# Optimization experiments

Hardware: AMD Instinct MI355X
Metric: run time of the kernel (lower is better)

Reference implementation:

```python
import jax, jax.numpy as jnp
import numpy as np

N_NODES = 50000
N_EDGES = 800000
G_DIM = 128
H1_DIM = 128
H2_DIM = 128
N_REL = 8          # 2 * n_speakers**2, n_speakers = 2
N_BASES = 30


def setup_inputs() -> dict:
    key = jax.random.key(0)
    ks = jax.random.split(key, 10)
    node_features = jax.random.normal(ks[0], (N_NODES, G_DIM), jnp.float32)
    edge_index = jax.random.randint(ks[1], (2, N_EDGES), 0, N_NODES, jnp.int32)
    edge_norm = jax.random.uniform(ks[2], (N_EDGES,), jnp.float32)
    edge_type = jax.random.randint(ks[3], (N_EDGES,), 0, N_REL, jnp.int32)
    # RGCN basis-decomposition params
    w_comp = jax.random.normal(ks[4], (N_REL, N_BASES), jnp.float32) / np.sqrt(N_BASES)
    bases = jax.random.normal(ks[5], (N_BASES, G_DIM, H1_DIM), jnp.float32) / np.sqrt(G_DIM)
    loop_weight = jax.random.normal(ks[6], (G_DIM, H1_DIM), jnp.float32) / np.sqrt(G_DIM)
    bias1 = jnp.zeros((H1_DIM,), jnp.float32)
    # GraphConv params
    W2 = jax.random.normal(ks[7], (H1_DIM, H2_DIM), jnp.float32) / np.sqrt(H1_DIM)
    bias2 = jnp.zeros((H2_DIM,), jnp.float32)
    return dict(node_features=node_features, edge_index=edge_index,
                edge_norm=edge_norm, edge_type=edge_type,
                w_comp=w_comp, bases=bases, loop_weight=loop_weight, bias1=bias1,
                W2=W2, bias2=bias2)


def reference(node_features, edge_index, edge_norm, edge_type,
              w_comp, bases, loop_weight, bias1, W2, bias2):
    N = node_features.shape[0]
    src, dst = edge_index[0], edge_index[1]

    # ---- RGCNConv (DGL RelGraphConv, basis regularizer, self_loop + bias) ----
    # relation weights from bases: [R, g, h1]
    weight = jnp.einsum('rb,bio->rio', w_comp, bases)
    # project all nodes by every relation (R is small), then gather per edge
    xw = jnp.einsum('ni,rio->rno', node_features, weight)   # [R, N, h1]
    msgs = xw[edge_type, src] * edge_norm[:, None]          # [E, h1]
    agg = jax.ops.segment_sum(msgs, dst, num_segments=N)    # scatter-add to dst
    h = agg + node_features @ loop_weight + bias1           # [N, h1]

    # ---- GraphConv (DGL, norm='both', edge_weight; degrees are UNweighted) ----
    ones = jnp.ones_like(edge_norm)
    out_deg = jax.ops.segment_sum(ones, src, num_segments=N)
    in_deg = jax.ops.segment_sum(ones, dst, num_segments=N)
    norm_src = jnp.clip(out_deg, 1.0) ** -0.5               # [N]
    norm_dst = jnp.clip(in_deg, 1.0) ** -0.5                # [N]
    m2 = (h * norm_src[:, None])[src] * edge_norm[:, None]  # [E, h1]
    agg2 = jax.ops.segment_sum(m2, dst, num_segments=N)     # [N, h1]
    out = (agg2 * norm_dst[:, None]) @ W2 + bias2           # [N, h2]
    return out
```

## Files before the change

kernel.cpp:

```cpp
#include <hip/hip_runtime.h>

#define NN 50000
#define EE 800000
#define NB 30
#define NJ 1152
#define NSB 49

typedef __attribute__((ext_vector_type(8))) short short8;
typedef __attribute__((ext_vector_type(4))) float f32x4;

__device__ __forceinline__ unsigned short f2bf(float f) {
  unsigned u = __float_as_uint(f);
  u += 0x7FFF + ((u >> 16) & 1);
  return (unsigned short)(u >> 16);
}
__device__ __forceinline__ float bf2f(unsigned short s) {
  return __uint_as_float(((unsigned)s) << 16);
}

__global__ void k_prep(const float* __restrict__ wcomp, const float* __restrict__ bases,
                       const float* __restrict__ loopw, const float* __restrict__ W2,
                       unsigned short* __restrict__ Wt, unsigned short* __restrict__ W2t) {
  int idx = blockIdx.x * 256 + threadIdx.x;
  if (idx < NJ * 128) {
    int j = idx >> 7, k = idx & 127;
    float v;
    if (j < 1024) {
      int r = j >> 7, o = j & 127;
      float s = 0.f;
#pragma unroll
      for (int b = 0; b < NB; ++b)
        s = fmaf(wcomp[r * NB + b], bases[((size_t)b * 128 + k) * 128 + o], s);
      v = s;
    } else {
      v = loopw[k * 128 + (j - 1024)];
    }
    Wt[idx] = f2bf(v);
  }
  if (idx < 128 * 128) {
    int j = idx >> 7, k = idx & 127;
    W2t[idx] = f2bf(W2[k * 128 + j]);
  }
}

__global__ void k_xbf(const float* __restrict__ X, unsigned short* __restrict__ Xbf) {
  int i = (blockIdx.x * 256 + threadIdx.x) * 4;
  float4 v = *(const float4*)(X + i);
  uint2 o;
  o.x = (unsigned)f2bf(v.x) | ((unsigned)f2bf(v.y) << 16);
  o.y = (unsigned)f2bf(v.z) | ((unsigned)f2bf(v.w) << 16);
  *(uint2*)(Xbf + i) = o;
}

__global__ void k_deg(const int* __restrict__ src, const int* __restrict__ dst,
                      int* __restrict__ dout, int* __restrict__ din) {
  int e = blockIdx.x * 256 + threadIdx.x;
  if (e < EE) {
    atomicAdd(&dout[src[e]], 1);
    atomicAdd(&din[dst[e]], 1);
  }
}

__global__ __launch_bounds__(256) void k_scan_a(const int* __restrict__ din,
                                                int* __restrict__ bsum) {
  __shared__ int wsum[4];
  int b = blockIdx.x, t = threadIdx.x;
  int lane = t & 63, w = t >> 6;
  int i0 = b * 1024 + t * 4;
  int s = 0;
  if (i0 + 3 < NN) {
    int4 d = *(const int4*)(din + i0);
    s = d.x + d.y + d.z + d.w;
  } else {
#pragma unroll
    for (int j = 0; j < 4; ++j) if (i0 + j < NN) s += din[i0 + j];
  }
#pragma unroll
  for (int off = 32; off; off >>= 1) s += __shfl_down(s, off, 64);
  if (lane == 0) wsum[w] = s;
  __syncthreads();
  if (t == 0) bsum[b] = wsum[0] + wsum[1] + wsum[2] + wsum[3];
}

__global__ void k_scan_b(int* __restrict__ bsum, int* __restrict__ row_ptr) {
  int t = threadIdx.x;
  int v = (t < NSB) ? bsum[t] : 0;
  int orig = v;
#pragma unroll
  for (int off = 1; off < 64; off <<= 1) {
    int u = __shfl_up(v, off, 64);
    if (t >= off) v += u;
  }
  if (t < NSB) bsum[t] = v - orig;
  if (t == 0) row_ptr[NN] = EE;
}

__global__ __launch_bounds__(256) void k_scan_c(const int* __restrict__ din,
                                                const int* __restrict__ bsum,
                                                int* __restrict__ row_ptr,
                                                int* __restrict__ cursor) {
  __shared__ int wsum[4];
  int b = blockIdx.x, t = threadIdx.x;
  int lane = t & 63, w = t >> 6;
  int i0 = b * 1024 + t * 4;
  int4 d = {0, 0, 0, 0};
  if (i0 + 3 < NN) {
    d = *(const int4*)(din + i0);
  } else {
    if (i0 + 0 < NN) d.x = din[i0 + 0];
    if (i0 + 1 < NN) d.y = din[i0 + 1];
    if (i0 + 2 < NN) d.z = din[i0 + 2];
  }
  int s = d.x + d.y + d.z + d.w;
  int v = s;
#pragma unroll
  for (int off = 1; off < 64; off <<= 1) {
    int u = __shfl_up(v, off, 64);
    if (lane >= off) v += u;
  }
  if (lane == 63) wsum[w] = v;
  __syncthreads();
  int woff = 0;
  for (int j = 0; j < w; ++j) woff += wsum[j];
  int base = bsum[b] + woff + (v - s);
  if (i0 + 0 < NN) { row_ptr[i0 + 0] = base; cursor[i0 + 0] = base; } base += d.x;
  if (i0 + 1 < NN) { row_ptr[i0 + 1] = base; cursor[i0 + 1] = base; } base += d.y;
  if (i0 + 2 < NN) { row_ptr[i0 + 2] = base; cursor[i0 + 2] = base; } base += d.z;
  if (i0 + 3 < NN) { row_ptr[i0 + 3] = base; cursor[i0 + 3] = base; }
}

__global__ void k_csr(const int* __restrict__ src, const int* __restrict__ dst,
                      const int* __restrict__ ety, const float* __restrict__ enorm,
                      int* __restrict__ cursor,
                      int2* __restrict__ em1, int2* __restrict__ em2) {
  int e = blockIdx.x * 256 + threadIdx.x;
  if (e < EE) {
    int pos = atomicAdd(&cursor[dst[e]], 1);
    int s = src[e];
    int wb = __float_as_int(enorm[e]);
    em1[pos] = make_int2(s * NJ + ety[e] * 128, wb);
    em2[pos] = make_int2(s * 128, wb);
  }
}

__global__ __launch_bounds__(256) void k_gemm(const unsigned short* __restrict__ A,
                                              const unsigned short* __restrict__ B,
                                              unsigned short* __restrict__ Cbf,
                                              float* __restrict__ Cf,
                                              const float* __restrict__ bias,
                                              int M, int ldc) {
  __shared__ unsigned short As[128 * 136];
  __shared__ unsigned short Bs[128 * 136];
  const int m0 = blockIdx.x * 128, j0 = blockIdx.y * 128;
  const int t = threadIdx.x;
  for (int i = t; i < 2048; i += 256) {
    int r = i >> 4, c = i & 15;
    uint4 va = {0, 0, 0, 0};
    int gr = m0 + r;
    if (gr < M) va = *(const uint4*)(A + (size_t)gr * 128 + c * 8);
    *(uint4*)(&As[r * 136 + c * 8]) = va;
    uint4 vb = *(const uint4*)(B + (size_t)(j0 + r) * 128 + c * 8);
    *(uint4*)(&Bs[r * 136 + c * 8]) = vb;
  }
  __syncthreads();

  const int lane = t & 63, wave = t >> 6;
  const int wr = (wave >> 1) * 64, wc = (wave & 1) * 64;
  const int lr = lane & 15, lk = (lane >> 4) * 8;

  f32x4 acc[4][4];
#pragma unroll
  for (int m = 0; m < 4; ++m)
#pragma unroll
    for (int n = 0; n < 4; ++n) acc[m][n] = (f32x4){0.f, 0.f, 0.f, 0.f};

#pragma unroll
  for (int kt = 0; kt < 4; ++kt) {
    short8 af[4], bfr[4];
#pragma unroll
    for (int m = 0; m < 4; ++m)
      af[m] = *(const short8*)(&As[(wr + m * 16 + lr) * 136 + kt * 32 + lk]);
#pragma unroll
    for (int n = 0; n < 4; ++n)
      bfr[n] = *(const short8*)(&Bs[(wc + n * 16 + lr) * 136 + kt * 32 + lk]);
#pragma unroll
    for (int m = 0; m < 4; ++m)
#pragma unroll
      for (int n = 0; n < 4; ++n)
        acc[m][n] = __builtin_amdgcn_mfma_f32_16x16x32_bf16(af[m], bfr[n], acc[m][n], 0, 0, 0);
  }

#pragma unroll
  for (int m = 0; m < 4; ++m) {
    int rbase = m0 + wr + m * 16 + (lane >> 4) * 4;
#pragma unroll
    for (int i = 0; i < 4; ++i) {
      int row = rbase + i;
      if (row >= M) continue;
      if (Cbf) {
        unsigned short* cr = Cbf + (size_t)row * ldc + j0 + wc;
#pragma unroll
        for (int n = 0; n < 4; ++n) cr[n * 16 + lr] = f2bf(acc[m][n][i]);
      } else {
        float* cr = Cf + (size_t)row * ldc + j0 + wc;
#pragma unroll
        for (int n = 0; n < 4; ++n) cr[n * 16 + lr] = acc[m][n][i] + bias[j0 + wc + n * 16 + lr];
      }
    }
  }
}

#define UNR 8

__global__ __launch_bounds__(256) void k_agg1(const unsigned short* __restrict__ xw,
                                              const int2* __restrict__ em1,
                                              const int* __restrict__ row_ptr,
                                              const int* __restrict__ deg_out,
                                              const float* __restrict__ bias1,
                                              unsigned short* __restrict__ hs) {
  int gw = (blockIdx.x * blockDim.x + threadIdx.x) >> 6;
  int lane = threadIdx.x & 63;
  if (gw >= NN) return;
  int beg = row_ptr[gw], end = row_ptr[gw + 1];
  float a0 = 0.f, a1 = 0.f;
  for (int i = beg; i < end; i += UNR) {
    int2 md[UNR];
    unsigned v[UNR];
#pragma unroll
    for (int j = 0; j < UNR; ++j) {
      int idx = i + j;
      idx = idx < end ? idx : end - 1;
      md[j] = em1[idx];
      if (i + j >= end) md[j].y = 0;
    }
#pragma unroll
    for (int j = 0; j < UNR; ++j)
      v[j] = *(const unsigned*)(xw + (size_t)(unsigned)md[j].x + lane * 2);
#pragma unroll
    for (int j = 0; j < UNR; ++j) {
      float w = __int_as_float(md[j].y);
      a0 = fmaf(w, bf2f((unsigned short)(v[j] & 0xffff)), a0);
      a1 = fmaf(w, bf2f((unsigned short)(v[j] >> 16)), a1);
    }
  }
  unsigned vl = *(const unsigned*)(xw + (size_t)gw * NJ + 1024 + lane * 2);
  float ns = rsqrtf(fmaxf((float)deg_out[gw], 1.f));
  float h0 = (a0 + bf2f((unsigned short)(vl & 0xffff)) + bias1[lane * 2]) * ns;
  float h1 = (a1 + bf2f((unsigned short)(vl >> 16)) + bias1[lane * 2 + 1]) * ns;
  unsigned o = (unsigned)f2bf(h0) | ((unsigned)f2bf(h1) << 16);
  *(unsigned*)(hs + (size_t)gw * 128 + lane * 2) = o;
}

__global__ __launch_bounds__(256) void k_agg2(const unsigned short* __restrict__ hs,
                                              const int2* __restrict__ em2,
                                              const int* __restrict__ row_ptr,
                                              unsigned short* __restrict__ zb) {
  int gw = (blockIdx.x * blockDim.x + threadIdx.x) >> 6;
  int lane = threadIdx.x & 63;
  if (gw >= NN) return;
  int beg = row_ptr[gw], end = row_ptr[gw + 1];
  float a0 = 0.f, a1 = 0.f;
  for (int i = beg; i < end; i += UNR) {
    int2 md[UNR];
    unsigned v[UNR];
#pragma unroll
    for (int j = 0; j < UNR; ++j) {
      int idx = i + j;
      idx = idx < end ? idx : end - 1;
      md[j] = em2[idx];
      if (i + j >= end) md[j].y = 0;
    }
#pragma unroll
    for (int j = 0; j < UNR; ++j)
      v[j] = *(const unsigned*)(hs + (size_t)(unsigned)md[j].x + lane * 2);
#pragma unroll
    for (int j = 0; j < UNR; ++j) {
      float w = __int_as_float(md[j].y);
      a0 = fmaf(w, bf2f((unsigned short)(v[j] & 0xffff)), a0);
      a1 = fmaf(w, bf2f((unsigned short)(v[j] >> 16)), a1);
    }
  }
  float nd = rsqrtf(fmaxf((float)(end - beg), 1.f));
  unsigned o = (unsigned)f2bf(a0 * nd) | ((unsigned)f2bf(a1 * nd) << 16);
  *(unsigned*)(zb + (size_t)gw * 128 + lane * 2) = o;
}

extern "C" void kernel_launch(void* const* d_in, const int* in_sizes, int n_in,
                              void* d_out, int out_size, void* d_ws, size_t ws_size,
                              hipStream_t stream) {
  const float* X = (const float*)d_in[0];
  const int* EI = (const int*)d_in[1];
  const float* enorm = (const float*)d_in[2];
  const int* etype = (const int*)d_in[3];
  const float* wcomp = (const float*)d_in[4];
  const float* bases = (const float*)d_in[5];
  const float* loopw = (const float*)d_in[6];
  const float* bias1 = (const float*)d_in[7];
  const float* W2 = (const float*)d_in[8];
  const float* bias2 = (const float*)d_in[9];
  float* out = (float*)d_out;
  const int* srcA = EI;
  const int* dstA = EI + EE;

  char* p = (char*)d_ws;
  auto alloc = [&](size_t bytes) {
    char* r = p;
    p += (bytes + 255) & ~(size_t)255;
    return r;
  };
  unsigned short* xw  = (unsigned short*)alloc((size_t)NN * NJ * 2);
  unsigned short* Xbf = (unsigned short*)alloc((size_t)NN * 128 * 2);
  unsigned short* hs  = (unsigned short*)alloc((size_t)NN * 128 * 2);
  unsigned short* zb  = (unsigned short*)alloc((size_t)NN * 128 * 2);
  unsigned short* Wt  = (unsigned short*)alloc((size_t)NJ * 128 * 2);
  unsigned short* W2t = (unsigned short*)alloc(128 * 128 * 2);
  int* deg     = (int*)alloc((size_t)2 * NN * 4);
  int* row_ptr = (int*)alloc((size_t)(NN + 1) * 4);
  int* cursor  = (int*)alloc((size_t)NN * 4);
  int* bsum    = (int*)alloc((size_t)NSB * 4);
  int2* em1    = (int2*)alloc((size_t)EE * 8);
  int2* em2    = (int2*)alloc((size_t)EE * 8);
  int* deg_out = deg;
  int* deg_in  = deg + NN;

  hipMemsetAsync(deg, 0, (size_t)2 * NN * sizeof(int), stream);
  hipLaunchKernelGGL(k_prep, dim3(576), dim3(256), 0, stream, wcomp, bases, loopw, W2, Wt, W2t);
  hipLaunchKernelGGL(k_xbf, dim3(6250), dim3(256), 0, stream, X, Xbf);
  hipLaunchKernelGGL(k_deg, dim3(3125), dim3(256), 0, stream, srcA, dstA, deg_out, deg_in);
  hipLaunchKernelGGL(k_scan_a, dim3(NSB), dim3(256), 0, stream, deg_in, bsum);
  hipLaunchKernelGGL(k_scan_b, dim3(1), dim3(64), 0, stream, bsum, row_ptr);
  hipLaunchKernelGGL(k_scan_c, dim3(NSB), dim3(256), 0, stream, deg_in, bsum, row_ptr, cursor);
  hipLaunchKernelGGL(k_csr, dim3(3125), dim3(256), 0, stream,
                     srcA, dstA, etype, enorm, cursor, em1, em2);
  hipLaunchKernelGGL(k_gemm, dim3(391, 9), dim3(256), 0, stream,
                     Xbf, Wt, xw, (float*)nullptr, (const float*)nullptr, NN, NJ);
  hipLaunchKernelGGL(k_agg1, dim3(12500), dim3(256), 0, stream,
                     xw, em1, row_ptr, deg_out, bias1, hs);
  hipLaunchKernelGGL(k_agg2, dim3(12500), dim3(256), 0, stream,
                     hs, em2, row_ptr, zb);
  hipLaunchKernelGGL(k_gemm, dim3(391, 1), dim3(256), 0, stream,
                     zb, W2t, (unsigned short*)nullptr, out, bias2, NN, 128);
}
```

Before: 386.9 us.

## Build degrees and CSR with LDS-partitioned histograms instead of global atomics

Replaces the global-atomic degree count and the cursor-based CSR fill with range-partitioned shared-memory histograms over edge slices. Per-slice partial counts are reduced in the first scan kernel, and a new scatter kernel derives per-slice cursors in LDS to place edges. This drops the memset and the contended global atomics. In exchange, every block rescans its whole edge slice, and the scatter kernel launches only 128 blocks, which limits parallelism.

```diff
diff --git a/kernel.cpp b/kernel.cpp
--- a/kernel.cpp
+++ b/kernel.cpp
@@ -5,6 +5,11 @@
 #define NB 30
 #define NJ 1152
 #define NSB 49
+#define NPART 16
+#define RANGE 3136
+#define NSLICE 8
+#define ESL 100000
+#define NPAD 50176
 
 typedef __attribute__((ext_vector_type(8))) short short8;
 typedef __attribute__((ext_vector_type(4))) float f32x4;
@@ -52,32 +57,55 @@
   *(uint2*)(Xbf + i) = o;
 }
 
-__global__ void k_deg(const int* __restrict__ src, const int* __restrict__ dst,
-                      int* __restrict__ dout, int* __restrict__ din) {
-  int e = blockIdx.x * 256 + threadIdx.x;
-  if (e < EE) {
-    atomicAdd(&dout[src[e]], 1);
-    atomicAdd(&din[dst[e]], 1);
-  }
-}
-
-__global__ __launch_bounds__(256) void k_scan_a(const int* __restrict__ din,
+__global__ __launch_bounds__(256) void k_hist(const int* __restrict__ EI,
+                                              int* __restrict__ pdin, int* __restrict__ pdout) {
+  __shared__ int hist[RANGE];
+  int b = blockIdx.x;
+  int kind = b & 1;
+  int sl = (b >> 1) & 7;
+  int r = b >> 4;
+  const int base = r * RANGE;
+  const int* vals = kind ? EI : EI + EE;
+  int* part = kind ? pdout : pdin;
+  for (int j = threadIdx.x; j < RANGE; j += 256) hist[j] = 0;
+  __syncthreads();
+  const int e0 = sl * ESL;
+  for (int i = threadIdx.x; i < ESL / 4; i += 256) {
+    int4 d = *(const int4*)(vals + e0 + i * 4);
+    int x;
+    x = d.x - base; if ((unsigned)x < RANGE) atomicAdd(&hist[x], 1);
+    x = d.y - base; if ((unsigned)x < RANGE) atomicAdd(&hist[x], 1);
+    x = d.z - base; if ((unsigned)x < RANGE) atomicAdd(&hist[x], 1);
+    x = d.w - base; if ((unsigned)x < RANGE) atomicAdd(&hist[x], 1);
+  }
+  __syncthreads();
+  for (int j = threadIdx.x; j < RANGE; j += 256)
+    part[sl * NPAD + base + j] = hist[j];
+}
+
+__global__ __launch_bounds__(256) void k_scan_a(const int* __restrict__ pdin,
+                                                const int* __restrict__ pdout,
+                                                int* __restrict__ din,
+                                                int* __restrict__ dout,
                                                 int* __restrict__ bsum) {
   __shared__ int wsum[4];
   int b = blockIdx.x, t = threadIdx.x;
   int lane = t & 63, w = t >> 6;
   int i0 = b * 1024 + t * 4;
-  int s = 0;
-  if (i0 + 3 < NN) {
-    int4 d = *(const int4*)(din + i0);
-    s = d.x + d.y + d.z + d.w;
-  } else {
-#pragma unroll
-    for (int j = 0; j < 4; ++j) if (i0 + j < NN) s += din[i0 + j];
-  }
-#pragma unroll
-  for (int off = 32; off; off >>= 1) s += __shfl_down(s, off, 64);
-  if (lane == 0) wsum[w] = s;
+  int4 acc = {0, 0, 0, 0}, od = {0, 0, 0, 0};
+#pragma unroll
+  for (int sl = 0; sl < NSLICE; ++sl) {
+    int4 a = *(const int4*)(pdin + sl * NPAD + i0);
+    int4 o = *(const int4*)(pdout + sl * NPAD + i0);
+    acc.x += a.x; acc.y += a.y; acc.z += a.z; acc.w += a.w;
+    od.x += o.x; od.y += o.y; od.z += o.z; od.w += o.w;
+  }
+  *(int4*)(din + i0) = acc;
+  *(int4*)(dout + i0) = od;
+  int sv = acc.x + acc.y + acc.z + acc.w;
+#pragma unroll
+  for (int off = 32; off; off >>= 1) sv += __shfl_down(sv, off, 64);
+  if (lane == 0) wsum[w] = sv;
   __syncthreads();
   if (t == 0) bsum[b] = wsum[0] + wsum[1] + wsum[2] + wsum[3];
 }
@@ -97,22 +125,14 @@
 
 __global__ __launch_bounds__(256) void k_scan_c(const int* __restrict__ din,
                                                 const int* __restrict__ bsum,
-                                                int* __restrict__ row_ptr,
-                                                int* __restrict__ cursor) {
+                                                int* __restrict__ row_ptr) {
   __shared__ int wsum[4];
   int b = blockIdx.x, t = threadIdx.x;
   int lane = t & 63, w = t >> 6;
   int i0 = b * 1024 + t * 4;
-  int4 d = {0, 0, 0, 0};
-  if (i0 + 3 < NN) {
-    d = *(const int4*)(din + i0);
-  } else {
-    if (i0 + 0 < NN) d.x = din[i0 + 0];
-    if (i0 + 1 < NN) d.y = din[i0 + 1];
-    if (i0 + 2 < NN) d.z = din[i0 + 2];
-  }
-  int s = d.x + d.y + d.z + d.w;
-  int v = s;
+  int4 d = *(const int4*)(din + i0);
+  int sth = d.x + d.y + d.z + d.w;
+  int v = sth;
 #pragma unroll
   for (int off = 1; off < 64; off <<= 1) {
     int u = __shfl_up(v, off, 64);
@@ -122,24 +142,47 @@
   __syncthreads();
   int woff = 0;
   for (int j = 0; j < w; ++j) woff += wsum[j];
-  int base = bsum[b] + woff + (v - s);
-  if (i0 + 0 < NN) { row_ptr[i0 + 0] = base; cursor[i0 + 0] = base; } base += d.x;
-  if (i0 + 1 < NN) { row_ptr[i0 + 1] = base; cursor[i0 + 1] = base; } base += d.y;
-  if (i0 + 2 < NN) { row_ptr[i0 + 2] = base; cursor[i0 + 2] = base; } base += d.z;
-  if (i0 + 3 < NN) { row_ptr[i0 + 3] = base; cursor[i0 + 3] = base; }
-}
-
-__global__ void k_csr(const int* __restrict__ src, const int* __restrict__ dst,
-                      const int* __restrict__ ety, const float* __restrict__ enorm,
-                      int* __restrict__ cursor,
-                      int2* __restrict__ em1, int2* __restrict__ em2) {
-  int e = blockIdx.x * 256 + threadIdx.x;
-  if (e < EE) {
-    int pos = atomicAdd(&cursor[dst[e]], 1);
-    int s = src[e];
-    int wb = __float_as_int(enorm[e]);
-    em1[pos] = make_int2(s * NJ + ety[e] * 128, wb);
-    em2[pos] = make_int2(s * 128, wb);
+  int base = bsum[b] + woff + (v - sth);
+  row_ptr[i0 + 0] = base; base += d.x;
+  row_ptr[i0 + 1] = base; base += d.y;
+  row_ptr[i0 + 2] = base; base += d.z;
+  row_ptr[i0 + 3] = base;
+}
+
+__global__ __launch_bounds__(256) void k_scatter(const int* __restrict__ src,
+                                                 const int* __restrict__ dst,
+                                                 const int* __restrict__ ety,
+                                                 const float* __restrict__ enorm,
+                                                 const int* __restrict__ pdin,
+                                                 const int* __restrict__ row_ptr,
+                                                 int2* __restrict__ em1,
+                                                 int2* __restrict__ em2) {
+  __shared__ int cur[RANGE];
+  int b = blockIdx.x;
+  int sl = b & 7, r = b >> 3;
+  const int base = r * RANGE;
+  for (int j = threadIdx.x; j < RANGE; j += 256) {
+    int off = row_ptr[base + j];
+    for (int sp = 0; sp < sl; ++sp) off += pdin[sp * NPAD + base + j];
+    cur[j] = off;
+  }
+  __syncthreads();
+  const int e0 = sl * ESL;
+  for (int i = threadIdx.x; i < ESL / 4; i += 256) {
+    int4 d = *(const int4*)(dst + e0 + i * 4);
+    int vals[4] = {d.x, d.y, d.z, d.w};
+#pragma unroll
+    for (int j = 0; j < 4; ++j) {
+      int dv = vals[j] - base;
+      if ((unsigned)dv < RANGE) {
+        int e = e0 + i * 4 + j;
+        int pos = atomicAdd(&cur[dv], 1);
+        int sv = src[e];
+        int wb = __float_as_int(enorm[e]);
+        em1[pos] = make_int2(sv * NJ + ety[e] * 128, wb);
+        em2[pos] = make_int2(sv * 128, wb);
+      }
+    }
   }
 }
 
@@ -314,28 +357,27 @@
   unsigned short* zb  = (unsigned short*)alloc((size_t)NN * 128 * 2);
   unsigned short* Wt  = (unsigned short*)alloc((size_t)NJ * 128 * 2);
   unsigned short* W2t = (unsigned short*)alloc(128 * 128 * 2);
-  int* deg     = (int*)alloc((size_t)2 * NN * 4);
-  int* row_ptr = (int*)alloc((size_t)(NN + 1) * 4);
-  int* cursor  = (int*)alloc((size_t)NN * 4);
+  int* pdin    = (int*)alloc((size_t)NSLICE * NPAD * 4);
+  int* pdout   = (int*)alloc((size_t)NSLICE * NPAD * 4);
+  int* din     = (int*)alloc((size_t)NPAD * 4);
+  int* dout    = (int*)alloc((size_t)NPAD * 4);
+  int* row_ptr = (int*)alloc((size_t)(NPAD + 1) * 4);
   int* bsum    = (int*)alloc((size_t)NSB * 4);
   int2* em1    = (int2*)alloc((size_t)EE * 8);
   int2* em2    = (int2*)alloc((size_t)EE * 8);
-  int* deg_out = deg;
-  int* deg_in  = deg + NN;
-
-  hipMemsetAsync(deg, 0, (size_t)2 * NN * sizeof(int), stream);
+
   hipLaunchKernelGGL(k_prep, dim3(576), dim3(256), 0, stream, wcomp, bases, loopw, W2, Wt, W2t);
   hipLaunchKernelGGL(k_xbf, dim3(6250), dim3(256), 0, stream, X, Xbf);
-  hipLaunchKernelGGL(k_deg, dim3(3125), dim3(256), 0, stream, srcA, dstA, deg_out, deg_in);
-  hipLaunchKernelGGL(k_scan_a, dim3(NSB), dim3(256), 0, stream, deg_in, bsum);
+  hipLaunchKernelGGL(k_hist, dim3(256), dim3(256), 0, stream, EI, pdin, pdout);
+  hipLaunchKernelGGL(k_scan_a, dim3(NSB), dim3(256), 0, stream, pdin, pdout, din, dout, bsum);
   hipLaunchKernelGGL(k_scan_b, dim3(1), dim3(64), 0, stream, bsum, row_ptr);
-  hipLaunchKernelGGL(k_scan_c, dim3(NSB), dim3(256), 0, stream, deg_in, bsum, row_ptr, cursor);
-  hipLaunchKernelGGL(k_csr, dim3(3125), dim3(256), 0, stream,
-                     srcA, dstA, etype, enorm, cursor, em1, em2);
+  hipLaunchKernelGGL(k_scan_c, dim3(NSB), dim3(256), 0, stream, din, bsum, row_ptr);
+  hipLaunchKernelGGL(k_scatter, dim3(128), dim3(256), 0, stream,
+                     srcA, dstA, etype, enorm, pdin, row_ptr, em1, em2);
   hipLaunchKernelGGL(k_gemm, dim3(391, 9), dim3(256), 0, stream,
                      Xbf, Wt, xw, (float*)nullptr, (const float*)nullptr, NN, NJ);
   hipLaunchKernelGGL(k_agg1, dim3(12500), dim3(256), 0, stream,
-                     xw, em1, row_ptr, deg_out, bias1, hs);
+                     xw, em1, row_ptr, dout, bias1, hs);
   hipLaunchKernelGGL(k_agg2, dim3(12500), dim3(256), 0, stream,
                      hs, em2, row_ptr, zb);
   hipLaunchKernelGGL(k_gemm, dim3(391, 1), dim3(256), 0, stream,
```

Result: slower. 479.5 us (+24.0%).
